# Optimization experiments

Measured on AMD Instinct MI355X. Metric: run time of the kernel, lower is better.

The kernel has to match this reference:

```python
import jax, jax.numpy as jnp
import numpy as np


def _unfold(x, k, stride, pad):
    """torch.nn.Unfold equivalent. x: [B,C,H,W] -> [B, C*k*k, L] with
    channel ordering (c, ki, kj) slow->fast and L = oh*ow row-major."""
    if pad:
        x = jnp.pad(x, ((0, 0), (0, 0), (pad, pad), (pad, pad)))
    B, C, H, W = x.shape
    oh = (H - k) // stride + 1
    ow = (W - k) // stride + 1
    r = jnp.arange(oh) * stride
    c = jnp.arange(ow) * stride
    xr = x[:, :, r[:, None] + jnp.arange(k)[None, :], :]          # [B,C,oh,k,W]
    xc = xr[:, :, :, :, c[:, None] + jnp.arange(k)[None, :]]      # [B,C,oh,ki,ow,kj]
    p = xc.transpose(0, 1, 3, 5, 2, 4)                            # [B,C,ki,kj,oh,ow]
    return p.reshape(B, C * k * k, oh * ow)


def _resize_bilinear(x, h, w):
    # matches F.interpolate(mode='bilinear', align_corners=False) for upsampling
    B, C = x.shape[0], x.shape[1]
    return jax.image.resize(x, (B, C, h, w), method='bilinear')


def setup_inputs() -> dict:
    key = jax.random.key(0)
    ks = jax.random.split(key, 8)
    bs, C, NC = 16, 768, 200
    x = jax.random.normal(ks[0], (bs, 784, C), jnp.float32)
    mask = jax.random.uniform(ks[1], (bs, 81), dtype=jnp.float32)
    img = jax.random.normal(ks[2], (bs, 3, 448, 448), jnp.float32)
    W_fc = jax.random.normal(ks[3], (NC, C), jnp.float32) * 0.02
    b_fc = jnp.zeros((NC,), jnp.float32)
    W_l = jax.random.normal(ks[4], (192, C), jnp.float32) * 0.02
    b_l = jnp.zeros((192,), jnp.float32)
    W_m = jax.random.normal(ks[5], (192, C), jnp.float32) * 0.02
    b_m = jnp.zeros((192,), jnp.float32)
    W_s = jax.random.normal(ks[6], (384, C), jnp.float32) * 0.02
    b_s = jnp.zeros((384,), jnp.float32)
    return dict(x=x, mask=mask, img=img, W_fc=W_fc, b_fc=b_fc,
                W_l=W_l, b_l=b_l, W_m=W_m, b_m=b_m, W_s=W_s, b_s=b_s)


def reference(x, mask, img, W_fc, b_fc, W_l, b_l, W_m, b_m, W_s, b_s):
    bs, C = x.shape[0], 768
    # im2col over image and feature map (all produce 81 = 9x9 windows)
    image_patches = _unfold(img, 128, 48, 32).transpose(0, 2, 1)   # [bs,81,3*128*128]
    feat = x.transpose(0, 2, 1).reshape(bs, C, 28, 28)
    patches_l = _unfold(feat, 8, 3, 2).transpose(0, 2, 1)          # [bs,81,C*64]
    patches_m = _unfold(feat, 6, 3, 1).transpose(0, 2, 1)          # [bs,81,C*36]
    patches_s = _unfold(feat, 4, 3, 0).transpose(0, 2, 1)          # [bs,81,C*16]
    # per-token class probabilities -> per-window importance score
    prob = jax.nn.softmax(x @ W_fc.T + b_fc, axis=-1)              # [bs,784,NC]
    max_logits = prob.max(axis=-1).reshape(bs, 1, 28, 28)
    part_logits = _unfold(max_logits, 8, 3, 2).mean(axis=1)        # [bs,81]
    part_logits = mask * part_logits
    sel = jnp.argmax(part_logits, axis=-1)                         # top-1 window id
    b_idx = jnp.arange(bs)
    parts_l = patches_l[b_idx, sel]                                # [bs,C*64]
    parts_m = patches_m[b_idx, sel]                                # [bs,C*36]
    parts_s = patches_s[b_idx, sel]                                # [bs,C*16]
    image_parts = image_patches[b_idx, sel]                        # [bs,3*128*128]
    # fold (single patch => reshape) + bilinear upsample to 8x8
    outl = parts_l.reshape(bs, C, 8, 8).transpose(0, 2, 3, 1).reshape(bs, 64, C)
    outm = _resize_bilinear(parts_m.reshape(bs, C, 6, 6), 8, 8)
    outm = outm.transpose(0, 2, 3, 1).reshape(bs, 64, C)
    outs = _resize_bilinear(parts_s.reshape(bs, C, 4, 4), 8, 8)
    outs = outs.transpose(0, 2, 3, 1).reshape(bs, 64, C)
    part1 = outl @ W_l.T + b_l                                     # [bs,64,192]
    part2 = outm @ W_m.T + b_m                                     # [bs,64,192]
    part3 = outs @ W_s.T + b_s                                     # [bs,64,384]
    ff_cat = jnp.concatenate([part1, part2, part3], axis=2)        # [bs,64,768]
    image_part = _resize_bilinear(image_parts.reshape(bs, 3, 128, 128), 224, 224)
    return ff_cat, image_part
```

## Files before the change

kernel.cpp:

```cpp
#include <hip/hip_runtime.h>
#include <math.h>

typedef __attribute__((ext_vector_type(8))) short bf16x8;
typedef __attribute__((ext_vector_type(4))) float f32x4;

__device__ __forceinline__ unsigned short f32_to_bf16_rne(float f) {
    unsigned int u = __float_as_uint(f);
    unsigned int r = (u + 0x7FFFu + ((u >> 16) & 1u)) >> 16;
    return (unsigned short)r;
}
__device__ __forceinline__ float bf16_to_f32(unsigned short h) {
    return __uint_as_float(((unsigned int)h) << 16);
}
__device__ __forceinline__ unsigned int pck(unsigned short a, unsigned short b) {
    return (unsigned int)a | ((unsigned int)b << 16);
}

__global__ __launch_bounds__(256) void k_wsplit(
    const float* __restrict__ Wfc, unsigned short* __restrict__ Whi,
    unsigned short* __restrict__ Wlo)
{
    const int idx = blockIdx.x * 256 + threadIdx.x;
    const int c = idx / 192;
    const int kk = (idx % 192) * 4;
    unsigned short h[4] = {0, 0, 0, 0}, l[4] = {0, 0, 0, 0};
    if (c < 200) {
        const float4 w = *(const float4*)&Wfc[c * 768 + kk];
        const float wv[4] = {w.x, w.y, w.z, w.w};
#pragma unroll
        for (int j = 0; j < 4; ++j) {
            h[j] = f32_to_bf16_rne(wv[j]);
            l[j] = f32_to_bf16_rne(wv[j] - bf16_to_f32(h[j]));
        }
    }
    *(uint2*)&Whi[c * 768 + kk] = make_uint2(pck(h[0], h[1]), pck(h[2], h[3]));
    *(uint2*)&Wlo[c * 768 + kk] = make_uint2(pck(l[0], l[1]), pck(l[2], l[3]));
}

__global__ __launch_bounds__(256) void k_logits(
    const float* __restrict__ x, const unsigned short* __restrict__ Whi,
    const unsigned short* __restrict__ Wlo, float* __restrict__ logits)
{
    __shared__ unsigned short Ah[4][64][8], Alo[4][64][8];
    __shared__ unsigned short Bh[8][64][8], Blo[8][64][8];
    const int tid = threadIdx.x;
    const int lane = tid & 63;
    const int wid = tid >> 6;
    const int wm = wid & 1, wn = wid >> 1;
    const int row0 = blockIdx.x * 64;
    const int n0 = blockIdx.y * 128;

    f32x4 acc[2][4];
    const f32x4 z = {0.f, 0.f, 0.f, 0.f};
#pragma unroll
    for (int mi = 0; mi < 2; ++mi)
#pragma unroll
        for (int q = 0; q < 4; ++q) acc[mi][q] = z;

    const int ar = tid & 63;
    const int ap = tid >> 6;
    const int bc = tid >> 1;
    const int bkh = tid & 1;

    for (int kc = 0; kc < 768; kc += 32) {
        __syncthreads();
        {
            const float* src = &x[(size_t)(row0 + ar) * 768 + kc + ap * 8];
            const float4 v0 = *(const float4*)src;
            const float4 v1 = *(const float4*)(src + 4);
            const float av[8] = {v0.x, v0.y, v0.z, v0.w, v1.x, v1.y, v1.z, v1.w};
            unsigned short h[8], l[8];
#pragma unroll
            for (int j = 0; j < 8; ++j) {
                h[j] = f32_to_bf16_rne(av[j]);
                l[j] = f32_to_bf16_rne(av[j] - bf16_to_f32(h[j]));
            }
            const int m = ar >> 4, ci = ar & 15;
            *(uint4*)&Ah[m][ap * 16 + ci][0] =
                make_uint4(pck(h[0], h[1]), pck(h[2], h[3]), pck(h[4], h[5]), pck(h[6], h[7]));
            *(uint4*)&Alo[m][ap * 16 + ci][0] =
                make_uint4(pck(l[0], l[1]), pck(l[2], l[3]), pck(l[4], l[5]), pck(l[6], l[7]));
        }
        {
            const size_t off = (size_t)(n0 + bc) * 768 + kc + bkh * 16;
            const uint4 h0 = *(const uint4*)&Whi[off];
            const uint4 h1 = *(const uint4*)&Whi[off + 8];
            const uint4 l0 = *(const uint4*)&Wlo[off];
            const uint4 l1 = *(const uint4*)&Wlo[off + 8];
            const int q = bc >> 4, ci = bc & 15;
            *(uint4*)&Bh[q][(2 * bkh) * 16 + ci][0] = h0;
            *(uint4*)&Bh[q][(2 * bkh + 1) * 16 + ci][0] = h1;
            *(uint4*)&Blo[q][(2 * bkh) * 16 + ci][0] = l0;
            *(uint4*)&Blo[q][(2 * bkh + 1) * 16 + ci][0] = l1;
        }
        __syncthreads();

        bf16x8 a_h[2], a_l[2];
#pragma unroll
        for (int mi = 0; mi < 2; ++mi) {
            a_h[mi] = *(const bf16x8*)&Ah[wm * 2 + mi][lane][0];
            a_l[mi] = *(const bf16x8*)&Alo[wm * 2 + mi][lane][0];
        }
#pragma unroll
        for (int q = 0; q < 4; ++q) {
            const bf16x8 bh = *(const bf16x8*)&Bh[wn * 4 + q][lane][0];
            const bf16x8 bl = *(const bf16x8*)&Blo[wn * 4 + q][lane][0];
#pragma unroll
            for (int mi = 0; mi < 2; ++mi) {
                acc[mi][q] = __builtin_amdgcn_mfma_f32_16x16x32_bf16(a_l[mi], bh, acc[mi][q], 0, 0, 0);
                acc[mi][q] = __builtin_amdgcn_mfma_f32_16x16x32_bf16(a_h[mi], bl, acc[mi][q], 0, 0, 0);
                acc[mi][q] = __builtin_amdgcn_mfma_f32_16x16x32_bf16(a_h[mi], bh, acc[mi][q], 0, 0, 0);
            }
        }
    }

#pragma unroll
    for (int mi = 0; mi < 2; ++mi)
#pragma unroll
        for (int q = 0; q < 4; ++q)
#pragma unroll
            for (int r = 0; r < 4; ++r) {
                const int row = row0 + wm * 32 + mi * 16 + (lane >> 4) * 4 + r;
                const int col = n0 + wn * 64 + q * 16 + (lane & 15);
                logits[(size_t)row * 256 + col] = acc[mi][q][r];
            }
}

__global__ __launch_bounds__(256) void k_softmax(
    const float* __restrict__ logits, const float* __restrict__ bfc,
    float* __restrict__ maxprob)
{
    const int row = blockIdx.x * 4 + (threadIdx.x >> 6);
    const int lane = threadIdx.x & 63;
    float v[4];
    float m = -1e30f;
#pragma unroll
    for (int j = 0; j < 4; ++j) {
        const int c = lane + j * 64;
        v[j] = (c < 200) ? (logits[(size_t)row * 256 + c] + bfc[c]) : -1e30f;
        m = fmaxf(m, v[j]);
    }
#pragma unroll
    for (int s = 32; s; s >>= 1) m = fmaxf(m, __shfl_xor(m, s, 64));
    float se = 0.f;
#pragma unroll
    for (int j = 0; j < 4; ++j) {
        const int c = lane + j * 64;
        if (c < 200) se += __expf(v[j] - m);
    }
#pragma unroll
    for (int s = 32; s; s >>= 1) se += __shfl_xor(se, s, 64);
    if (lane == 0) maxprob[row] = 1.0f / se;
}

__global__ void k_sel(const float* __restrict__ maxprob,
                      const float* __restrict__ mask, int* __restrict__ sel)
{
    __shared__ float mp[784];
    __shared__ float pl[81];
    const int b = blockIdx.x, tid = threadIdx.x;
    for (int i = tid; i < 784; i += blockDim.x) mp[i] = maxprob[b * 784 + i];
    __syncthreads();
    if (tid < 81) {
        const int pr = tid / 9, pc = tid % 9;
        float s = 0.f;
        for (int ki = 0; ki < 8; ++ki) {
            const int y = pr * 3 - 2 + ki;
            if (y < 0 || y >= 28) continue;
            for (int kj = 0; kj < 8; ++kj) {
                const int xx = pc * 3 - 2 + kj;
                if (xx < 0 || xx >= 28) continue;
                s += mp[y * 28 + xx];
            }
        }
        pl[tid] = mask[b * 81 + tid] * (s * (1.f / 64.f));
    }
    __syncthreads();
    if (tid == 0) {
        float best = pl[0]; int bi = 0;
        for (int i = 1; i < 81; ++i) if (pl[i] > best) { best = pl[i]; bi = i; }
        sel[b] = bi;
    }
}

__device__ __forceinline__ void rcoef8(int o, int n, int& f0, int& f1, float& w)
{
    float s = (o + 0.5f) * ((float)n * 0.125f) - 0.5f;
    s = fminf(fmaxf(s, 0.f), (float)(n - 1));
    f0 = (int)s;
    w = s - (float)f0;
    f1 = f0 + 1; if (f1 > n - 1) f1 = n - 1;
}

__global__ __launch_bounds__(256) void k_build(
    const float* __restrict__ x, const int* __restrict__ sel,
    float* __restrict__ Al, float* __restrict__ Am, float* __restrict__ As)
{
    __shared__ float W8[64][256];
    const int b = blockIdx.x / 3;
    const int tid = threadIdx.x;
    const int c = (blockIdx.x % 3) * 256 + tid;
    const int s = sel[b];
    const int y0 = (s / 9) * 3 - 2, x0 = (s % 9) * 3 - 2;

#pragma unroll 4
    for (int p = 0; p < 64; ++p) {
        const int yy = y0 + (p >> 3), xx = x0 + (p & 7);
        float v = 0.f;
        if (yy >= 0 && yy < 28 && xx >= 0 && xx < 28)
            v = x[((size_t)b * 784 + yy * 28 + xx) * 768 + c];
        W8[p][tid] = v;
    }
    __syncthreads();

#pragma unroll 4
    for (int p = 0; p < 64; ++p)
        Al[((size_t)b * 64 + p) * 768 + c] = W8[p][tid];

    {
        int f0[8], f1[8]; float w[8];
        for (int o = 0; o < 8; ++o) rcoef8(o, 6, f0[o], f1[o], w[o]);
        for (int oy = 0; oy < 8; ++oy)
            for (int ox = 0; ox < 8; ++ox) {
                const float g00 = W8[(1 + f0[oy]) * 8 + 1 + f0[ox]][tid];
                const float g01 = W8[(1 + f0[oy]) * 8 + 1 + f1[ox]][tid];
                const float g10 = W8[(1 + f1[oy]) * 8 + 1 + f0[ox]][tid];
                const float g11 = W8[(1 + f1[oy]) * 8 + 1 + f1[ox]][tid];
                const float v0 = g00 + w[ox] * (g01 - g00);
                const float v1 = g10 + w[ox] * (g11 - g10);
                Am[((size_t)b * 64 + oy * 8 + ox) * 768 + c] = v0 + w[oy] * (v1 - v0);
            }
    }
    {
        int f0[8], f1[8]; float w[8];
        for (int o = 0; o < 8; ++o) rcoef8(o, 4, f0[o], f1[o], w[o]);
        for (int oy = 0; oy < 8; ++oy)
            for (int ox = 0; ox < 8; ++ox) {
                const float g00 = W8[(2 + f0[oy]) * 8 + 2 + f0[ox]][tid];
                const float g01 = W8[(2 + f0[oy]) * 8 + 2 + f1[ox]][tid];
                const float g10 = W8[(2 + f1[oy]) * 8 + 2 + f0[ox]][tid];
                const float g11 = W8[(2 + f1[oy]) * 8 + 2 + f1[ox]][tid];
                const float v0 = g00 + w[ox] * (g01 - g00);
                const float v1 = g10 + w[ox] * (g11 - g10);
                As[((size_t)b * 64 + oy * 8 + ox) * 768 + c] = v0 + w[oy] * (v1 - v0);
            }
    }
}

__global__ __launch_bounds__(256) void k_gemm(
    const float* __restrict__ Al, const float* __restrict__ Am, const float* __restrict__ As,
    const float* __restrict__ Wl, const float* __restrict__ bl,
    const float* __restrict__ Wm, const float* __restrict__ bm,
    const float* __restrict__ Ws, const float* __restrict__ bs_,
    float* __restrict__ out)
{
    __shared__ float At[64][36];
    __shared__ float Wt[64][36];
    const int blk = blockIdx.x;
    const int b = blk / 12, t = blk % 12;
    const float* A; const float* W; const float* bias;
    if (t < 3)      { A = Al; W = Wl + (size_t)t       * 64 * 768; bias = bl  + t * 64; }
    else if (t < 6) { A = Am; W = Wm + (size_t)(t - 3) * 64 * 768; bias = bm  + (t - 3) * 64; }
    else            { A = As; W = Ws + (size_t)(t - 6) * 64 * 768; bias = bs_ + (t - 6) * 64; }
    A += (size_t)b * 64 * 768;
    const int n0 = t * 64;
    const int tid = threadIdx.x;
    const int ti = tid >> 4, tn = tid & 15;
    const int lr = tid >> 2;
    const int lc = (tid & 3) * 8;

    float acc[4][4];
#pragma unroll
    for (int r = 0; r < 4; ++r)
#pragma unroll
        for (int q = 0; q < 4; ++q) acc[r][q] = 0.f;

    for (int kc = 0; kc < 768; kc += 32) {
        __syncthreads();
        *(float4*)&At[lr][lc]     = *(const float4*)&A[(size_t)lr * 768 + kc + lc];
        *(float4*)&At[lr][lc + 4] = *(const float4*)&A[(size_t)lr * 768 + kc + lc + 4];
        *(float4*)&Wt[lr][lc]     = *(const float4*)&W[(size_t)lr * 768 + kc + lc];
        *(float4*)&Wt[lr][lc + 4] = *(const float4*)&W[(size_t)lr * 768 + kc + lc + 4];
        __syncthreads();
#pragma unroll
        for (int k4 = 0; k4 < 32; k4 += 4) {
            float4 a[4], w[4];
#pragma unroll
            for (int r = 0; r < 4; ++r) a[r] = *(const float4*)&At[ti + 16 * r][k4];
#pragma unroll
            for (int q = 0; q < 4; ++q) w[q] = *(const float4*)&Wt[tn + 16 * q][k4];
#pragma unroll
            for (int r = 0; r < 4; ++r)
#pragma unroll
                for (int q = 0; q < 4; ++q)
                    acc[r][q] += a[r].x * w[q].x + a[r].y * w[q].y
                               + a[r].z * w[q].z + a[r].w * w[q].w;
        }
    }
#pragma unroll
    for (int r = 0; r < 4; ++r)
#pragma unroll
        for (int q = 0; q < 4; ++q)
            out[((size_t)b * 64 + ti + 16 * r) * 768 + n0 + tn + 16 * q]
                = acc[r][q] + bias[tn + 16 * q];
}

__global__ __launch_bounds__(256) void k_image(
    const float* __restrict__ img, const int* __restrict__ sel,
    float* __restrict__ out)
{
    const int idx = blockIdx.x * 256 + threadIdx.x;
    if (idx >= 16 * 3 * 224 * 224) return;
    const int ox = idx % 224;
    int t = idx / 224;
    const int oy = t % 224; t /= 224;
    const int c = t % 3;
    const int b = t / 3;
    const int s = sel[b];
    const int ry0 = (s / 9) * 48 - 32, cx0 = (s % 9) * 48 - 32;

    float sy = (oy + 0.5f) * (128.f / 224.f) - 0.5f;
    sy = fminf(fmaxf(sy, 0.f), 127.f);
    const int fy0 = (int)sy; const float wy = sy - (float)fy0;
    const int fy1 = (fy0 < 127) ? fy0 + 1 : 127;

    float sx = (ox + 0.5f) * (128.f / 224.f) - 0.5f;
    sx = fminf(fmaxf(sx, 0.f), 127.f);
    const int fx0 = (int)sx; const float wx = sx - (float)fx0;
    const int fx1 = (fx0 < 127) ? fx0 + 1 : 127;

    const float* ib = img + ((size_t)b * 3 + c) * 448 * 448;
    auto rd = [&](int py, int px) -> float {
        const int r = ry0 + py, cc = cx0 + px;
        return (r >= 0 && r < 448 && cc >= 0 && cc < 448) ? ib[r * 448 + cc] : 0.f;
    };
    const float g00 = rd(fy0, fx0), g01 = rd(fy0, fx1);
    const float g10 = rd(fy1, fx0), g11 = rd(fy1, fx1);
    const float v0 = g00 + wx * (g01 - g00);
    const float v1 = g10 + wx * (g11 - g10);
    out[idx] = v0 + wy * (v1 - v0);
}

extern "C" void kernel_launch(void* const* d_in, const int* in_sizes, int n_in,
                              void* d_out, int out_size, void* d_ws, size_t ws_size,
                              hipStream_t stream)
{
    const float* x    = (const float*)d_in[0];
    const float* mask = (const float*)d_in[1];
    const float* img  = (const float*)d_in[2];
    const float* Wfc  = (const float*)d_in[3];
    const float* bfc  = (const float*)d_in[4];
    const float* Wl   = (const float*)d_in[5];
    const float* bl   = (const float*)d_in[6];
    const float* Wm   = (const float*)d_in[7];
    const float* bm   = (const float*)d_in[8];
    const float* Ws   = (const float*)d_in[9];
    const float* bs   = (const float*)d_in[10];
    float* out = (float*)d_out;

    char* ws = (char*)d_ws;
    float* maxprob        = (float*)ws;
    int*   sel            = (int*)(ws + 51200);
    unsigned short* Whi   = (unsigned short*)(ws + 65536);
    unsigned short* Wlo   = (unsigned short*)(ws + 65536 + 393216);
    float* logits = (float*)(ws + 1048576);
    float* Al     = (float*)(ws + 1048576);
    float* Am     = Al + (size_t)16 * 64 * 768;
    float* As     = Am + (size_t)16 * 64 * 768;

    hipLaunchKernelGGL(k_wsplit,  dim3(192),      dim3(256), 0, stream, Wfc, Whi, Wlo);
    hipLaunchKernelGGL(k_logits,  dim3(196, 2),   dim3(256), 0, stream, x, Whi, Wlo, logits);
    hipLaunchKernelGGL(k_softmax, dim3(3136),     dim3(256), 0, stream, logits, bfc, maxprob);
    hipLaunchKernelGGL(k_sel,     dim3(16),       dim3(128), 0, stream, maxprob, mask, sel);
    hipLaunchKernelGGL(k_build,   dim3(48),       dim3(256), 0, stream, x, sel, Al, Am, As);
    hipLaunchKernelGGL(k_gemm,    dim3(192),      dim3(256), 0, stream,
                       Al, Am, As, Wl, bl, Wm, bm, Ws, bs, out);
    hipLaunchKernelGGL(k_image,   dim3(9408),     dim3(256), 0, stream,
                       img, sel, out + 786432);
}
```

Baseline: 245.4 us.

## Fuse patch build and resize into MFMA split-bf16 projection GEMM

Removes the separate build kernel that wrote the Al/Am/As intermediates. The projection GEMM now gathers the selected 8x8 window from x per k-chunk, computes the bilinear resize inline, splits the result into bf16 hi/lo parts and runs three bf16 MFMAs per tile instead of the scalar fp32 FMA loop. The projection weights are pre-split into hi/lo bf16 by three extra split launches. This cuts the intermediate global writes and reads plus one launch, but adds weight-split work on every call and a third barrier per k-step. It also drops the lo*lo term, which slightly lowers precision.

Result: faster. 215.9 us (-12.0%).

```diff
diff --git a/kernel.cpp b/kernel.cpp
--- a/kernel.cpp
+++ b/kernel.cpp
@@ -16,16 +16,17 @@
     return (unsigned int)a | ((unsigned int)b << 16);
 }
 
-__global__ __launch_bounds__(256) void k_wsplit(
-    const float* __restrict__ Wfc, unsigned short* __restrict__ Whi,
-    unsigned short* __restrict__ Wlo)
+__global__ __launch_bounds__(256) void k_split(
+    const float* __restrict__ src, unsigned short* __restrict__ hi,
+    unsigned short* __restrict__ lo, int src_rows, int nq)
 {
     const int idx = blockIdx.x * 256 + threadIdx.x;
+    if (idx >= nq) return;
     const int c = idx / 192;
     const int kk = (idx % 192) * 4;
     unsigned short h[4] = {0, 0, 0, 0}, l[4] = {0, 0, 0, 0};
-    if (c < 200) {
-        const float4 w = *(const float4*)&Wfc[c * 768 + kk];
+    if (c < src_rows) {
+        const float4 w = *(const float4*)&src[(size_t)c * 768 + kk];
         const float wv[4] = {w.x, w.y, w.z, w.w};
 #pragma unroll
         for (int j = 0; j < 4; ++j) {
@@ -33,8 +34,8 @@
             l[j] = f32_to_bf16_rne(wv[j] - bf16_to_f32(h[j]));
         }
     }
-    *(uint2*)&Whi[c * 768 + kk] = make_uint2(pck(h[0], h[1]), pck(h[2], h[3]));
-    *(uint2*)&Wlo[c * 768 + kk] = make_uint2(pck(l[0], l[1]), pck(l[2], l[3]));
+    *(uint2*)&hi[(size_t)c * 768 + kk] = make_uint2(pck(h[0], h[1]), pck(h[2], h[3]));
+    *(uint2*)&lo[(size_t)c * 768 + kk] = make_uint2(pck(l[0], l[1]), pck(l[2], l[3]));
 }
 
 __global__ __launch_bounds__(256) void k_logits(
@@ -192,117 +193,131 @@
     f1 = f0 + 1; if (f1 > n - 1) f1 = n - 1;
 }
 
-__global__ __launch_bounds__(256) void k_build(
+__global__ __launch_bounds__(256) void k_ff(
     const float* __restrict__ x, const int* __restrict__ sel,
-    float* __restrict__ Al, float* __restrict__ Am, float* __restrict__ As)
-{
-    __shared__ float W8[64][256];
-    const int b = blockIdx.x / 3;
-    const int tid = threadIdx.x;
-    const int c = (blockIdx.x % 3) * 256 + tid;
-    const int s = sel[b];
-    const int y0 = (s / 9) * 3 - 2, x0 = (s % 9) * 3 - 2;
-
-#pragma unroll 4
-    for (int p = 0; p < 64; ++p) {
-        const int yy = y0 + (p >> 3), xx = x0 + (p & 7);
-        float v = 0.f;
-        if (yy >= 0 && yy < 28 && xx >= 0 && xx < 28)
-            v = x[((size_t)b * 784 + yy * 28 + xx) * 768 + c];
-        W8[p][tid] = v;
-    }
-    __syncthreads();
-
-#pragma unroll 4
-    for (int p = 0; p < 64; ++p)
-        Al[((size_t)b * 64 + p) * 768 + c] = W8[p][tid];
-
-    {
-        int f0[8], f1[8]; float w[8];
-        for (int o = 0; o < 8; ++o) rcoef8(o, 6, f0[o], f1[o], w[o]);
-        for (int oy = 0; oy < 8; ++oy)
-            for (int ox = 0; ox < 8; ++ox) {
-                const float g00 = W8[(1 + f0[oy]) * 8 + 1 + f0[ox]][tid];
-                const float g01 = W8[(1 + f0[oy]) * 8 + 1 + f1[ox]][tid];
-                const float g10 = W8[(1 + f1[oy]) * 8 + 1 + f0[ox]][tid];
-                const float g11 = W8[(1 + f1[oy]) * 8 + 1 + f1[ox]][tid];
-                const float v0 = g00 + w[ox] * (g01 - g00);
-                const float v1 = g10 + w[ox] * (g11 - g10);
-                Am[((size_t)b * 64 + oy * 8 + ox) * 768 + c] = v0 + w[oy] * (v1 - v0);
-            }
-    }
-    {
-        int f0[8], f1[8]; float w[8];
-        for (int o = 0; o < 8; ++o) rcoef8(o, 4, f0[o], f1[o], w[o]);
-        for (int oy = 0; oy < 8; ++oy)
-            for (int ox = 0; ox < 8; ++ox) {
-                const float g00 = W8[(2 + f0[oy]) * 8 + 2 + f0[ox]][tid];
-                const float g01 = W8[(2 + f0[oy]) * 8 + 2 + f1[ox]][tid];
-                const float g10 = W8[(2 + f1[oy]) * 8 + 2 + f0[ox]][tid];
-                const float g11 = W8[(2 + f1[oy]) * 8 + 2 + f1[ox]][tid];
-                const float v0 = g00 + w[ox] * (g01 - g00);
-                const float v1 = g10 + w[ox] * (g11 - g10);
-                As[((size_t)b * 64 + oy * 8 + ox) * 768 + c] = v0 + w[oy] * (v1 - v0);
-            }
-    }
-}
-
-__global__ __launch_bounds__(256) void k_gemm(
-    const float* __restrict__ Al, const float* __restrict__ Am, const float* __restrict__ As,
-    const float* __restrict__ Wl, const float* __restrict__ bl,
-    const float* __restrict__ Wm, const float* __restrict__ bm,
-    const float* __restrict__ Ws, const float* __restrict__ bs_,
-    float* __restrict__ out)
-{
-    __shared__ float At[64][36];
-    __shared__ float Wt[64][36];
+    const unsigned short* __restrict__ Whi2, const unsigned short* __restrict__ Wlo2,
+    const float* __restrict__ bl, const float* __restrict__ bm,
+    const float* __restrict__ bs_, float* __restrict__ out)
+{
+    __shared__ float W8[64][33];
+    __shared__ unsigned short Ah[4][64][8], Alo[4][64][8];
+    __shared__ unsigned short Bh[4][64][8], Blo[4][64][8];
+
     const int blk = blockIdx.x;
     const int b = blk / 12, t = blk % 12;
-    const float* A; const float* W; const float* bias;
-    if (t < 3)      { A = Al; W = Wl + (size_t)t       * 64 * 768; bias = bl  + t * 64; }
-    else if (t < 6) { A = Am; W = Wm + (size_t)(t - 3) * 64 * 768; bias = bm  + (t - 3) * 64; }
-    else            { A = As; W = Ws + (size_t)(t - 6) * 64 * 768; bias = bs_ + (t - 6) * 64; }
-    A += (size_t)b * 64 * 768;
     const int n0 = t * 64;
+    const int seg = (t < 3) ? 0 : ((t < 6) ? 1 : 2);
+    const float* bias = (seg == 0) ? (bl + t * 64)
+                      : (seg == 1) ? (bm + (t - 3) * 64)
+                                   : (bs_ + (t - 6) * 64);
+    const int s = sel[b];
+    const int wy0 = (s / 9) * 3 - 2, wx0 = (s % 9) * 3 - 2;
+
     const int tid = threadIdx.x;
-    const int ti = tid >> 4, tn = tid & 15;
-    const int lr = tid >> 2;
-    const int lc = (tid & 3) * 8;
-
-    float acc[4][4];
-#pragma unroll
-    for (int r = 0; r < 4; ++r)
-#pragma unroll
-        for (int q = 0; q < 4; ++q) acc[r][q] = 0.f;
+    const int lane = tid & 63;
+    const int wid = tid >> 6, wmi = wid & 1, wn = wid >> 1;
+
+    const int gp = tid & 63;
+    const int gy = wy0 + (gp >> 3), gx = wx0 + (gp & 7);
+    const bool inb = (gy >= 0 && gy < 28 && gx >= 0 && gx < 28);
+    const float* xsrc = x + ((size_t)b * 784 + (inb ? (gy * 28 + gx) : 0)) * 768;
+    const int ko = (tid >> 6) * 8;
+
+    const int ai = tid & 63;
+    int r00, r01, r10, r11; float fx = 0.f, fy = 0.f;
+    if (seg == 0) { r00 = r01 = r10 = r11 = ai; }
+    else {
+        const int nn = (seg == 1) ? 6 : 4, off = (seg == 1) ? 1 : 2;
+        int f0y, f1y, f0x, f1x;
+        rcoef8(ai >> 3, nn, f0y, f1y, fy);
+        rcoef8(ai & 7, nn, f0x, f1x, fx);
+        r00 = (off + f0y) * 8 + off + f0x;
+        r01 = (off + f0y) * 8 + off + f1x;
+        r10 = (off + f1y) * 8 + off + f0x;
+        r11 = (off + f1y) * 8 + off + f1x;
+    }
+
+    const int bc = tid >> 2, kq = tid & 3;
+    const unsigned short* WhP = Whi2 + (size_t)(n0 + bc) * 768 + kq * 8;
+    const unsigned short* WlP = Wlo2 + (size_t)(n0 + bc) * 768 + kq * 8;
+
+    f32x4 acc[2][2];
+    const f32x4 z = {0.f, 0.f, 0.f, 0.f};
+#pragma unroll
+    for (int mi = 0; mi < 2; ++mi)
+#pragma unroll
+        for (int q = 0; q < 2; ++q) acc[mi][q] = z;
 
     for (int kc = 0; kc < 768; kc += 32) {
         __syncthreads();
-        *(float4*)&At[lr][lc]     = *(const float4*)&A[(size_t)lr * 768 + kc + lc];
-        *(float4*)&At[lr][lc + 4] = *(const float4*)&A[(size_t)lr * 768 + kc + lc + 4];
-        *(float4*)&Wt[lr][lc]     = *(const float4*)&W[(size_t)lr * 768 + kc + lc];
-        *(float4*)&Wt[lr][lc + 4] = *(const float4*)&W[(size_t)lr * 768 + kc + lc + 4];
-        __syncthreads();
-#pragma unroll
-        for (int k4 = 0; k4 < 32; k4 += 4) {
-            float4 a[4], w[4];
-#pragma unroll
-            for (int r = 0; r < 4; ++r) a[r] = *(const float4*)&At[ti + 16 * r][k4];
-#pragma unroll
-            for (int q = 0; q < 4; ++q) w[q] = *(const float4*)&Wt[tn + 16 * q][k4];
-#pragma unroll
-            for (int r = 0; r < 4; ++r)
-#pragma unroll
-                for (int q = 0; q < 4; ++q)
-                    acc[r][q] += a[r].x * w[q].x + a[r].y * w[q].y
-                               + a[r].z * w[q].z + a[r].w * w[q].w;
-        }
-    }
-#pragma unroll
-    for (int r = 0; r < 4; ++r)
-#pragma unroll
-        for (int q = 0; q < 4; ++q)
-            out[((size_t)b * 64 + ti + 16 * r) * 768 + n0 + tn + 16 * q]
-                = acc[r][q] + bias[tn + 16 * q];
+        {
+            float v[8] = {0, 0, 0, 0, 0, 0, 0, 0};
+            if (inb) {
+                const float4 a0 = *(const float4*)(xsrc + kc + ko);
+                const float4 a1 = *(const float4*)(xsrc + kc + ko + 4);
+                v[0] = a0.x; v[1] = a0.y; v[2] = a0.z; v[3] = a0.w;
+                v[4] = a1.x; v[5] = a1.y; v[6] = a1.z; v[7] = a1.w;
+            }
+#pragma unroll
+            for (int j = 0; j < 8; ++j) W8[gp][ko + j] = v[j];
+        }
+        {
+            const uint4 h = *(const uint4*)(WhP + kc);
+            const uint4 l = *(const uint4*)(WlP + kc);
+            *(uint4*)&Bh[bc >> 4][kq * 16 + (bc & 15)][0] = h;
+            *(uint4*)&Blo[bc >> 4][kq * 16 + (bc & 15)][0] = l;
+        }
+        __syncthreads();
+        {
+            unsigned short h[8], l[8];
+#pragma unroll
+            for (int j = 0; j < 8; ++j) {
+                const int k = ko + j;
+                const float g00 = W8[r00][k], g01 = W8[r01][k];
+                const float g10 = W8[r10][k], g11 = W8[r11][k];
+                const float v0 = g00 + fx * (g01 - g00);
+                const float v1 = g10 + fx * (g11 - g10);
+                const float a = v0 + fy * (v1 - v0);
+                h[j] = f32_to_bf16_rne(a);
+                l[j] = f32_to_bf16_rne(a - bf16_to_f32(h[j]));
+            }
+            const int m = ai >> 4, ci = ai & 15, p2 = ko >> 3;
+            *(uint4*)&Ah[m][p2 * 16 + ci][0] =
+                make_uint4(pck(h[0], h[1]), pck(h[2], h[3]), pck(h[4], h[5]), pck(h[6], h[7]));
+            *(uint4*)&Alo[m][p2 * 16 + ci][0] =
+                make_uint4(pck(l[0], l[1]), pck(l[2], l[3]), pck(l[4], l[5]), pck(l[6], l[7]));
+        }
+        __syncthreads();
+
+        bf16x8 a_h[2], a_l[2];
+#pragma unroll
+        for (int mi = 0; mi < 2; ++mi) {
+            a_h[mi] = *(const bf16x8*)&Ah[wmi * 2 + mi][lane][0];
+            a_l[mi] = *(const bf16x8*)&Alo[wmi * 2 + mi][lane][0];
+        }
+#pragma unroll
+        for (int q = 0; q < 2; ++q) {
+            const bf16x8 bh = *(const bf16x8*)&Bh[wn * 2 + q][lane][0];
+            const bf16x8 bl2 = *(const bf16x8*)&Blo[wn * 2 + q][lane][0];
+#pragma unroll
+            for (int mi = 0; mi < 2; ++mi) {
+                acc[mi][q] = __builtin_amdgcn_mfma_f32_16x16x32_bf16(a_l[mi], bh, acc[mi][q], 0, 0, 0);
+                acc[mi][q] = __builtin_amdgcn_mfma_f32_16x16x32_bf16(a_h[mi], bl2, acc[mi][q], 0, 0, 0);
+                acc[mi][q] = __builtin_amdgcn_mfma_f32_16x16x32_bf16(a_h[mi], bh, acc[mi][q], 0, 0, 0);
+            }
+        }
+    }
+
+#pragma unroll
+    for (int mi = 0; mi < 2; ++mi)
+#pragma unroll
+        for (int q = 0; q < 2; ++q)
+#pragma unroll
+            for (int r = 0; r < 4; ++r) {
+                const int row = wmi * 32 + mi * 16 + (lane >> 4) * 4 + r;
+                const int col = wn * 32 + q * 16 + (lane & 15);
+                out[((size_t)b * 64 + row) * 768 + n0 + col] = acc[mi][q][r] + bias[col];
+            }
 }
 
 __global__ __launch_bounds__(256) void k_image(
@@ -359,22 +374,26 @@
     float* out = (float*)d_out;
 
     char* ws = (char*)d_ws;
-    float* maxprob        = (float*)ws;
-    int*   sel            = (int*)(ws + 51200);
-    unsigned short* Whi   = (unsigned short*)(ws + 65536);
-    unsigned short* Wlo   = (unsigned short*)(ws + 65536 + 393216);
-    float* logits = (float*)(ws + 1048576);
-    float* Al     = (float*)(ws + 1048576);
-    float* Am     = Al + (size_t)16 * 64 * 768;
-    float* As     = Am + (size_t)16 * 64 * 768;
-
-    hipLaunchKernelGGL(k_wsplit,  dim3(192),      dim3(256), 0, stream, Wfc, Whi, Wlo);
-    hipLaunchKernelGGL(k_logits,  dim3(196, 2),   dim3(256), 0, stream, x, Whi, Wlo, logits);
-    hipLaunchKernelGGL(k_softmax, dim3(3136),     dim3(256), 0, stream, logits, bfc, maxprob);
-    hipLaunchKernelGGL(k_sel,     dim3(16),       dim3(128), 0, stream, maxprob, mask, sel);
-    hipLaunchKernelGGL(k_build,   dim3(48),       dim3(256), 0, stream, x, sel, Al, Am, As);
-    hipLaunchKernelGGL(k_gemm,    dim3(192),      dim3(256), 0, stream,
-                       Al, Am, As, Wl, bl, Wm, bm, Ws, bs, out);
-    hipLaunchKernelGGL(k_image,   dim3(9408),     dim3(256), 0, stream,
+    float* maxprob      = (float*)ws;
+    int*   sel          = (int*)(ws + 51200);
+    unsigned short* Whi  = (unsigned short*)(ws + 65536);
+    unsigned short* Wlo  = (unsigned short*)(ws + 65536 + 393216);
+    unsigned short* Whi2 = (unsigned short*)(ws + 917504);
+    unsigned short* Wlo2 = (unsigned short*)(ws + 917504 + 1179648);
+    float* logits = (float*)(ws + 3276800);
+
+    hipLaunchKernelGGL(k_split, dim3(192), dim3(256), 0, stream, Wfc, Whi, Wlo, 200, 256 * 192);
+    hipLaunchKernelGGL(k_split, dim3(144), dim3(256), 0, stream, Wl, Whi2, Wlo2, 192, 192 * 192);
+    hipLaunchKernelGGL(k_split, dim3(144), dim3(256), 0, stream,
+                       Wm, Whi2 + (size_t)192 * 768, Wlo2 + (size_t)192 * 768, 192, 192 * 192);
+    hipLaunchKernelGGL(k_split, dim3(288), dim3(256), 0, stream,
+                       Ws, Whi2 + (size_t)384 * 768, Wlo2 + (size_t)384 * 768, 384, 384 * 192);
+
+    hipLaunchKernelGGL(k_logits,  dim3(196, 2), dim3(256), 0, stream, x, Whi, Wlo, logits);
+    hipLaunchKernelGGL(k_softmax, dim3(3136),   dim3(256), 0, stream, logits, bfc, maxprob);
+    hipLaunchKernelGGL(k_sel,     dim3(16),     dim3(128), 0, stream, maxprob, mask, sel);
+    hipLaunchKernelGGL(k_ff,      dim3(192),    dim3(256), 0, stream,
+                       x, sel, Whi2, Wlo2, bl, bm, bs, out);
+    hipLaunchKernelGGL(k_image,   dim3(9408),   dim3(256), 0, stream,
                        img, sel, out + 786432);
 }
```
